# Performance work log

Hardware: AMD Instinct MI355X
Metric: run time of the kernel (lower is better)

Reference implementation:

```python
import jax, jax.numpy as jnp
import numpy as np

WS = 512   # window_size
LB = 1     # look_backward
LF = 1     # look_forward
H = 16     # num_attention_heads
NC = LB + LF + 1  # concatenated windows per query window


def _collect(a, pad_value):
    # a: [B, nw, ws, ...]; gather windows [i-LB, i+LF] for each window i,
    # padding the window axis with pad_value (faithful to collect_windows).
    nw = a.shape[1]
    pads = [(0, 0), (LB, LF)] + [(0, 0)] * (a.ndim - 2)
    ap = jnp.pad(a, pads, constant_values=pad_value)
    idx = jnp.arange(nw)[:, None] + jnp.arange(NC)[None, :]  # [nw, NC]
    g = ap[:, idx]  # [B, nw, NC, ws, ...]
    return g.reshape(g.shape[0], nw, NC * a.shape[2], *a.shape[3:])


def setup_inputs() -> dict:
    key = jax.random.key(0)
    ks = jax.random.split(key, 9)
    B, S, E = 1, 4096, 1024
    x = jax.random.normal(ks[0], (B, S, E), dtype=jnp.float32)
    std = 0.02
    wq = std * jax.random.normal(ks[1], (E, E), dtype=jnp.float32)
    wk = std * jax.random.normal(ks[2], (E, E), dtype=jnp.float32)
    wv = std * jax.random.normal(ks[3], (E, E), dtype=jnp.float32)
    wo = std * jax.random.normal(ks[4], (E, E), dtype=jnp.float32)
    bq = std * jax.random.normal(ks[5], (E,), dtype=jnp.float32)
    bk = std * jax.random.normal(ks[6], (E,), dtype=jnp.float32)
    bv = std * jax.random.normal(ks[7], (E,), dtype=jnp.float32)
    bo = std * jax.random.normal(ks[8], (E,), dtype=jnp.float32)
    return {"x": x, "wq": wq, "bq": bq, "wk": wk, "bk": bk,
            "wv": wv, "bv": bv, "wo": wo, "bo": bo}


def reference(x, wq, bq, wk, bk, wv, bv, wo, bo):
    B, S, E = x.shape
    hd = E // H
    nw = S // WS  # seq_len chosen divisible by window_size

    def proj(w, b):
        y = x @ w.T + b
        return y.reshape(B, S, H, hd).transpose(0, 2, 1, 3).reshape(B * H, S, hd)

    q = proj(wq, bq)
    k = proj(wk, bk)
    v = proj(wv, bv)

    qb = q.reshape(B * H, nw, WS, hd)
    # NOTE: original pads K/V window buffers with value -1 (not zero); pad
    # positions are NOT masked (the `!= -1` clause excludes them) -- replicated.
    kb = _collect(k.reshape(B * H, nw, WS, hd), -1.0)  # [BH, nw, NC*WS, hd]
    vb = _collect(v.reshape(B * H, nw, WS, hd), -1.0)

    t = jnp.arange(S, dtype=jnp.int32).reshape(1, nw, WS)
    ct = _collect(t, -1)  # [1, nw, NC*WS] key positions (-1 for pads)

    # Unscaled QK^T (original applies no 1/sqrt(d)).
    scores = jnp.einsum('bwqd,bwkd->bwqk', qb, kb)  # [BH, nw, WS, NC*WS]

    qi = t.reshape(1, nw, WS, 1)          # query absolute positions
    ctb = ct[:, :, None, :]               # key absolute positions
    over = ((ctb > qi + WS * LF) | (ctb < qi - WS * LB)) & (ctb != -1)
    scores = jnp.where(over, -jnp.inf, scores)

    attn = jax.nn.softmax(scores, axis=-1)
    out = jnp.einsum('bwqk,bwkd->bwqd', attn, vb)  # [BH, nw, WS, hd]
    out = out.reshape(B, H, S, hd).transpose(0, 2, 1, 3).reshape(B, S, E)
    return out @ wo.T + bo
```

## Files before the change

kernel.cpp:

```cpp
#include <hip/hip_runtime.h>
#include <stdint.h>

#define S 4096
#define E 1024
#define NH 16
#define HD 64
#define WSZ 512

typedef _Float16 f16x8 __attribute__((ext_vector_type(8)));
typedef _Float16 f16x4 __attribute__((ext_vector_type(4)));
typedef float f32x4 __attribute__((ext_vector_type(4)));
typedef unsigned short u16;
typedef unsigned int u32;

__device__ __forceinline__ u16 f2h_bits(float f) {
    union { _Float16 h; u16 u; } cv; cv.h = (_Float16)f; return cv.u;
}

__device__ __forceinline__ void gld16(const u16* g, u16* l) {
    __builtin_amdgcn_global_load_lds((const __attribute__((address_space(1))) void*)g,
                                     (__attribute__((address_space(3))) void*)l, 16, 0, 0);
}

struct CvtArgs {
    const float* s[5];
    u16* d[5];
    int n[5];
};
__global__ void cvt5(CvtArgs a) {
    int seg = blockIdx.y;
    const float* __restrict__ s = a.s[seg];
    u16* __restrict__ d = a.d[seg];
    int n = a.n[seg];
    for (int i = (blockIdx.x * 256 + threadIdx.x) * 4; i < n; i += gridDim.x * 1024) {
        float4 f = *(const float4*)&s[i];
        uint2 o;
        o.x = (u32)f2h_bits(f.x) | ((u32)f2h_bits(f.y) << 16);
        o.y = (u32)f2h_bits(f.z) | ((u32)f2h_bits(f.w) << 16);
        *(uint2*)&d[i] = o;
    }
}

__global__ __launch_bounds__(256) void gemm_qkv(
    const u16* __restrict__ A, const u16* __restrict__ B,
    u16* __restrict__ OutQK, u16* __restrict__ OutVT,
    const float* __restrict__ b0, const float* __restrict__ b1, const float* __restrict__ b2,
    int K) {
    __shared__ __align__(16) u16 As[128 * 32];
    __shared__ __align__(16) u16 Bs[128 * 32];
    const int tid = threadIdx.x;
    const int wid = tid >> 6, lid = tid & 63, quad = lid >> 4, l16 = lid & 15;
    const int wm = wid >> 1, wn = wid & 1;
    const int bm0 = blockIdx.x * 128, bn0 = blockIdx.y * 128;

    f32x4 acc[4][4] = {};
    const int sr = tid >> 2, sc = (tid & 3) * 8;

    for (int k0 = 0; k0 < K; k0 += 32) {
        __syncthreads();
        gld16(&A[(size_t)(bm0 + sr) * K + k0 + sc],      &As[tid * 8]);
        gld16(&A[(size_t)(bm0 + sr + 64) * K + k0 + sc], &As[2048 + tid * 8]);
        gld16(&B[(size_t)(bn0 + sr) * K + k0 + sc],      &Bs[tid * 8]);
        gld16(&B[(size_t)(bn0 + sr + 64) * K + k0 + sc], &Bs[2048 + tid * 8]);
        __syncthreads();
        f16x8 af[4], bf[4];
#pragma unroll
        for (int i = 0; i < 4; ++i) af[i] = *(const f16x8*)&As[(wm * 64 + i * 16 + l16) * 32 + quad * 8];
#pragma unroll
        for (int j = 0; j < 4; ++j) bf[j] = *(const f16x8*)&Bs[(wn * 64 + j * 16 + l16) * 32 + quad * 8];
#pragma unroll
        for (int i = 0; i < 4; ++i)
#pragma unroll
            for (int j = 0; j < 4; ++j)
                acc[i][j] = __builtin_amdgcn_mfma_f32_16x16x32_f16(af[i], bf[j], acc[i][j], 0, 0, 0);
    }

    const bool isV = (bn0 >= 2048);
#pragma unroll
    for (int j = 0; j < 4; ++j) {
        int n = bn0 + wn * 64 + j * 16 + l16;
        float bias = (n < 1024) ? b0[n] : (n < 2048 ? b1[n - 1024] : b2[n - 2048]);
#pragma unroll
        for (int i = 0; i < 4; ++i) {
            int m0 = bm0 + wm * 64 + i * 16 + quad * 4;
            if (!isV) {
#pragma unroll
                for (int r = 0; r < 4; ++r)
                    OutQK[(size_t)(m0 + r) * 2048 + n] = f2h_bits(acc[i][j][r] + bias);
            } else {
                u16 h0 = f2h_bits(acc[i][j][0] + bias);
                u16 h1 = f2h_bits(acc[i][j][1] + bias);
                u16 h2 = f2h_bits(acc[i][j][2] + bias);
                u16 h3 = f2h_bits(acc[i][j][3] + bias);
                uint2 pk;
                pk.x = (u32)h0 | ((u32)h1 << 16);
                pk.y = (u32)h2 | ((u32)h3 << 16);
                *(uint2*)&OutVT[(size_t)(n - 2048) * 4096 + m0] = pk;
            }
        }
    }
}

__global__ __launch_bounds__(256) void gemm_n64(
    const u16* __restrict__ A, const u16* __restrict__ B, float* __restrict__ OutF,
    const float* __restrict__ bias, int N, int K) {
    __shared__ __align__(16) u16 As[128 * 32];
    __shared__ __align__(16) u16 Bs[64 * 32];
    const int tid = threadIdx.x;
    const int wid = tid >> 6, lid = tid & 63, quad = lid >> 4, l16 = lid & 15;
    const int bm0 = blockIdx.x * 128, bn0 = blockIdx.y * 64;

    f32x4 acc[2][4] = {};
    const int sr = tid >> 2, sc = (tid & 3) * 8;

    for (int k0 = 0; k0 < K; k0 += 32) {
        __syncthreads();
        gld16(&A[(size_t)(bm0 + sr) * K + k0 + sc],      &As[tid * 8]);
        gld16(&A[(size_t)(bm0 + sr + 64) * K + k0 + sc], &As[2048 + tid * 8]);
        gld16(&B[(size_t)(bn0 + sr) * K + k0 + sc],      &Bs[tid * 8]);
        __syncthreads();
        f16x8 af[2], bf[4];
#pragma unroll
        for (int i = 0; i < 2; ++i) af[i] = *(const f16x8*)&As[(wid * 32 + i * 16 + l16) * 32 + quad * 8];
#pragma unroll
        for (int j = 0; j < 4; ++j) bf[j] = *(const f16x8*)&Bs[(j * 16 + l16) * 32 + quad * 8];
#pragma unroll
        for (int i = 0; i < 2; ++i)
#pragma unroll
            for (int j = 0; j < 4; ++j)
                acc[i][j] = __builtin_amdgcn_mfma_f32_16x16x32_f16(af[i], bf[j], acc[i][j], 0, 0, 0);
    }

#pragma unroll
    for (int j = 0; j < 4; ++j) {
        int n = bn0 + j * 16 + l16;
        float bv = bias[n];
#pragma unroll
        for (int i = 0; i < 2; ++i) {
            int m0 = bm0 + wid * 32 + i * 16 + quad * 4;
#pragma unroll
            for (int r = 0; r < 4; ++r)
                OutF[(size_t)(m0 + r) * N + n] = acc[i][j][r] + bv;
        }
    }
}

__global__ __launch_bounds__(512, 4) void attn_win(const u16* __restrict__ QK, const u16* __restrict__ VT,
                                                   u16* __restrict__ AO) {
    const int qt = blockIdx.x, w = blockIdx.y, h = blockIdx.z;
    const int tid = threadIdx.x, wid = tid >> 6, lid = tid & 63, quad = lid >> 4, l16 = lid & 15;

    __shared__ __align__(16) u16 Ks[2][64 * 32];
    __shared__ __align__(16) u16 Vt[2][64 * 36];

    const int qrow = w * WSZ + qt * 128 + wid * 16 + l16;
    const _Float16 L2E = (_Float16)1.44269504f;
    f16x8 qf[2];
#pragma unroll
    for (int ks = 0; ks < 2; ++ks) {
        qf[ks] = *(const f16x8*)&QK[(size_t)qrow * 2048 + h * 64 + ks * 32 + quad * 8];
#pragma unroll
        for (int j = 0; j < 8; ++j) qf[ks][j] *= L2E;
    }

    const int npad = (w == 0 || w == 7) ? 512 : 0;
    float s_p = 0.f;
    if (npad) {
        float sq = 0.f;
#pragma unroll
        for (int j = 0; j < 8; ++j) sq += (float)qf[0][j] + (float)qf[1][j];
        sq += __shfl_xor(sq, 16, 64);
        sq += __shfl_xor(sq, 32, 64);
        s_p = -sq;
    }

    f32x4 oacc[4] = {};
    float mrun = -30000.f;
    float lsum = 0.f;

    const int g0base = (w - 1) * WSZ;
    const int rqloc = qt * 128 + wid * 16 + l16;
    const int rqw0 = qt * 128 + wid * 16;

    const int kst = tid & 255, kkh = tid >> 8;
    const int vd = tid >> 3, vk0 = (tid & 7) * 8;

    for (int c = 0; c < 24; ++c) {
        const int g0 = g0base + c * 64;
        if (g0 < 0 || g0 >= S) continue;
        if (!((c * 64 + 63 >= qt * 128) && (c * 64 <= qt * 128 + 1151))) continue;

        __syncthreads();
        gld16(QK + (size_t)(g0 + (kst >> 2)) * 2048 + 1024 + h * 64 + kkh * 32 + (kst & 3) * 8,
              &Ks[0][0] + kkh * 2048 + kst * 8);
        {
            uint4 va = *(const uint4*)(VT + (size_t)(h * 64 + vd) * 4096 + g0 + vk0);
            u16* vp = &Vt[vk0 >> 5][vd * 36 + (vk0 & 31)];
            *(uint2*)(vp)     = make_uint2(va.x, va.y);
            *(uint2*)(vp + 4) = make_uint2(va.z, va.w);
        }
        __syncthreads();

        f32x4 sc[4];
#pragma unroll
        for (int nt = 0; nt < 4; ++nt) {
            f16x8 kf0 = *(const f16x8*)&Ks[0][(nt * 16 + l16) * 32 + quad * 8];
            f16x8 kf1 = *(const f16x8*)&Ks[1][(nt * 16 + l16) * 32 + quad * 8];
            f32x4 t = {};
            t = __builtin_amdgcn_mfma_f32_16x16x32_f16(kf0, qf[0], t, 0, 0, 0);
            t = __builtin_amdgcn_mfma_f32_16x16x32_f16(kf1, qf[1], t, 0, 0, 0);
            sc[nt] = t;
        }

        const bool needs_mask = (c * 64 < rqw0 + 16) || (c * 64 + 63 > rqw0 + 1024);
        if (needs_mask) {
#pragma unroll
            for (int nt = 0; nt < 4; ++nt)
#pragma unroll
                for (int r = 0; r < 4; ++r) {
                    int n = c * 64 + nt * 16 + quad * 4 + r;
                    if (n < rqloc || n > rqloc + 1024) sc[nt][r] = -30000.f;
                }
        }

        float mloc = mrun;
#pragma unroll
        for (int nt = 0; nt < 4; ++nt)
            mloc = fmaxf(mloc, fmaxf(fmaxf(sc[nt][0], sc[nt][1]), fmaxf(sc[nt][2], sc[nt][3])));
        mloc = fmaxf(mloc, __shfl_xor(mloc, 16, 64));
        mloc = fmaxf(mloc, __shfl_xor(mloc, 32, 64));

        const bool up = __any(mloc > mrun);
        float ls = 0.f;
        f16x4 pf[4];
#pragma unroll
        for (int nt = 0; nt < 4; ++nt)
#pragma unroll
            for (int r = 0; r < 4; ++r) {
                float p = exp2f(sc[nt][r] - mloc);
                ls += p;
                pf[nt][r] = (_Float16)p;
            }
        if (up) {
            float alpha = exp2f(mrun - mloc);
            mrun = mloc;
            lsum = lsum * alpha + ls;
            float ao[4];
#pragma unroll
            for (int r = 0; r < 4; ++r) ao[r] = __shfl(alpha, quad * 4 + r, 64);
#pragma unroll
            for (int dt = 0; dt < 4; ++dt)
#pragma unroll
                for (int r = 0; r < 4; ++r) oacc[dt][r] *= ao[r];
        } else {
            lsum += ls;
        }

#pragma unroll
        for (int nt = 0; nt < 4; ++nt)
#pragma unroll
            for (int dt = 0; dt < 4; ++dt) {
                f16x4 vf = *(const f16x4*)&Vt[nt >> 1][(dt * 16 + l16) * 36 + (nt & 1) * 16 + quad * 4];
                oacc[dt] = __builtin_amdgcn_mfma_f32_16x16x16f16(pf[nt], vf, oacc[dt], 0, 0, 0);
            }
    }

    float lt = lsum;
    lt += __shfl_xor(lt, 16, 64);
    lt += __shfl_xor(lt, 32, 64);
    float aW = 1.f, pw = 0.f;
    if (npad) {
        float mnew = fmaxf(mrun, s_p);
        aW = exp2f(mrun - mnew);
        pw = 512.f * exp2f(s_p - mnew);
        lt = lt * aW + pw;
    }
    float linv = 1.f / lt;
    float lrec[4], arow[4], pwrow[4];
#pragma unroll
    for (int r = 0; r < 4; ++r) {
        lrec[r]  = __shfl(linv, quad * 4 + r, 64);
        arow[r]  = __shfl(aW,   quad * 4 + r, 64);
        pwrow[r] = __shfl(pw,   quad * 4 + r, 64);
    }
#pragma unroll
    for (int dt = 0; dt < 4; ++dt)
#pragma unroll
        for (int r = 0; r < 4; ++r) {
            int srow = w * WSZ + qt * 128 + wid * 16 + quad * 4 + r;
            int col = h * 64 + dt * 16 + l16;
            float o = (oacc[dt][r] * arow[r] - pwrow[r]) * lrec[r];
            AO[(size_t)srow * E + col] = f2h_bits(o);
        }
}

extern "C" void kernel_launch(void* const* d_in, const int* in_sizes, int n_in,
                              void* d_out, int out_size, void* d_ws, size_t ws_size,
                              hipStream_t stream) {
    const float* x  = (const float*)d_in[0];
    const float* wq = (const float*)d_in[1];
    const float* bq = (const float*)d_in[2];
    const float* wk = (const float*)d_in[3];
    const float* bk = (const float*)d_in[4];
    const float* wv = (const float*)d_in[5];
    const float* bv = (const float*)d_in[6];
    const float* wo = (const float*)d_in[7];
    const float* bo = (const float*)d_in[8];
    float* out = (float*)d_out;

    char* ws = (char*)d_ws;
    u16* XH  = (u16*)(ws);
    u16* WC  = (u16*)(ws + 8388608);
    u16* WOh = (u16*)(ws + 14680064);
    u16* QK  = (u16*)(ws + 16777216);
    u16* VTg = (u16*)(ws + 33554432);
    u16* AOh = (u16*)(ws + 41943040);

    CvtArgs ca;
    ca.s[0] = x;  ca.d[0] = XH;            ca.n[0] = 4194304;
    ca.s[1] = wq; ca.d[1] = WC;            ca.n[1] = 1048576;
    ca.s[2] = wk; ca.d[2] = WC + 1048576;  ca.n[2] = 1048576;
    ca.s[3] = wv; ca.d[3] = WC + 2097152;  ca.n[3] = 1048576;
    ca.s[4] = wo; ca.d[4] = WOh;           ca.n[4] = 1048576;
    cvt5<<<dim3(1024, 5), 256, 0, stream>>>(ca);

    gemm_qkv<<<dim3(32, 24), 256, 0, stream>>>(XH, WC, QK, VTg, bq, bk, bv, 1024);
    attn_win<<<dim3(4, 8, 16), 512, 0, stream>>>(QK, VTg, AOh);
    gemm_n64<<<dim3(32, 16), 256, 0, stream>>>(AOh, WOh, out, bo, 1024, 1024);
}
```

Before: 198.1 us.

## Double-buffer K/V tiles in windowed attention and precompute chunk loop bounds

```diff
diff --git a/kernel.cpp b/kernel.cpp
--- a/kernel.cpp
+++ b/kernel.cpp
@@ -150,8 +150,8 @@
     const int qt = blockIdx.x, w = blockIdx.y, h = blockIdx.z;
     const int tid = threadIdx.x, wid = tid >> 6, lid = tid & 63, quad = lid >> 4, l16 = lid & 15;
 
-    __shared__ __align__(16) u16 Ks[2][64 * 32];
-    __shared__ __align__(16) u16 Vt[2][64 * 36];
+    __shared__ __align__(16) u16 Ks[2][2 * 64 * 32];
+    __shared__ __align__(16) u16 Vt[2][2 * 64 * 36];
 
     const int qrow = w * WSZ + qt * 128 + wid * 16 + l16;
     const _Float16 L2E = (_Float16)1.44269504f;
@@ -182,30 +182,45 @@
     const int rqloc = qt * 128 + wid * 16 + l16;
     const int rqw0 = qt * 128 + wid * 16;
 
+    int cfirst = 2 * qt; if ((1 - w) * 8 > cfirst) cfirst = (1 - w) * 8;
+    int clast = 2 * qt + 17; if (71 - 8 * w < clast) clast = 71 - 8 * w; if (clast > 23) clast = 23;
+
     const int kst = tid & 255, kkh = tid >> 8;
     const int vd = tid >> 3, vk0 = (tid & 7) * 8;
-
-    for (int c = 0; c < 24; ++c) {
-        const int g0 = g0base + c * 64;
-        if (g0 < 0 || g0 >= S) continue;
-        if (!((c * 64 + 63 >= qt * 128) && (c * 64 <= qt * 128 + 1151))) continue;
-
-        __syncthreads();
-        gld16(QK + (size_t)(g0 + (kst >> 2)) * 2048 + 1024 + h * 64 + kkh * 32 + (kst & 3) * 8,
-              &Ks[0][0] + kkh * 2048 + kst * 8);
-        {
-            uint4 va = *(const uint4*)(VT + (size_t)(h * 64 + vd) * 4096 + g0 + vk0);
-            u16* vp = &Vt[vk0 >> 5][vd * 36 + (vk0 & 31)];
-            *(uint2*)(vp)     = make_uint2(va.x, va.y);
-            *(uint2*)(vp + 4) = make_uint2(va.z, va.w);
-        }
-        __syncthreads();
+    const size_t kgoff = 1024 + h * 64 + kkh * 32 + (kst & 3) * 8 + (size_t)(kst >> 2) * 2048;
+    const int kloff = kkh * 2048 + kst * 8;
+    const u16* vgrow = VT + (size_t)(h * 64 + vd) * 4096 + vk0;
+    const int vloff = (vk0 >> 5) * 2304 + vd * 36 + (vk0 & 31);
+
+    {
+        const int g0 = g0base + cfirst * 64;
+        uint4 va = *(const uint4*)(vgrow + g0);
+        gld16(QK + (size_t)g0 * 2048 + kgoff, &Ks[0][0] + kloff);
+        u16* vp = &Vt[0][0] + vloff;
+        *(uint2*)(vp)     = make_uint2(va.x, va.y);
+        *(uint2*)(vp + 4) = make_uint2(va.z, va.w);
+    }
+
+    int ib = 0;
+    for (int c = cfirst; c <= clast; ++c, ib ^= 1) {
+        __syncthreads();
+
+        const bool has_next = (c < clast);
+        uint4 vnext;
+        if (has_next) {
+            const int gn = g0base + (c + 1) * 64;
+            vnext = *(const uint4*)(vgrow + gn);
+            gld16(QK + (size_t)gn * 2048 + kgoff, &Ks[ib ^ 1][0] + kloff);
+        }
+
+        const u16* KsB = &Ks[ib][0];
+        const u16* VtB = &Vt[ib][0];
 
         f32x4 sc[4];
 #pragma unroll
         for (int nt = 0; nt < 4; ++nt) {
-            f16x8 kf0 = *(const f16x8*)&Ks[0][(nt * 16 + l16) * 32 + quad * 8];
-            f16x8 kf1 = *(const f16x8*)&Ks[1][(nt * 16 + l16) * 32 + quad * 8];
+            f16x8 kf0 = *(const f16x8*)&KsB[(nt * 16 + l16) * 32 + quad * 8];
+            f16x8 kf1 = *(const f16x8*)&KsB[2048 + (nt * 16 + l16) * 32 + quad * 8];
             f32x4 t = {};
             t = __builtin_amdgcn_mfma_f32_16x16x32_f16(kf0, qf[0], t, 0, 0, 0);
             t = __builtin_amdgcn_mfma_f32_16x16x32_f16(kf1, qf[1], t, 0, 0, 0);
@@ -260,9 +275,15 @@
         for (int nt = 0; nt < 4; ++nt)
 #pragma unroll
             for (int dt = 0; dt < 4; ++dt) {
-                f16x4 vf = *(const f16x4*)&Vt[nt >> 1][(dt * 16 + l16) * 36 + (nt & 1) * 16 + quad * 4];
+                f16x4 vf = *(const f16x4*)&VtB[(nt >> 1) * 2304 + (dt * 16 + l16) * 36 + (nt & 1) * 16 + quad * 4];
                 oacc[dt] = __builtin_amdgcn_mfma_f32_16x16x16f16(pf[nt], vf, oacc[dt], 0, 0, 0);
             }
+
+        if (has_next) {
+            u16* vp = &Vt[ib ^ 1][0] + vloff;
+            *(uint2*)(vp)     = make_uint2(vnext.x, vnext.y);
+            *(uint2*)(vp + 4) = make_uint2(vnext.z, vnext.w);
+        }
     }
 
     float lt = lsum;
```

Measured after the change: 196.5 us. No clear change (-0.8%).
